# Kernel optimization log

Hardware: AMD Instinct MI355X
Metric: run time of the kernel (lower is better)

The kernel has to match this reference:

```python
import jax, jax.numpy as jnp
import numpy as np

N = 100_000      # nodes
E = 1_600_000    # edges (avg degree 16)
D_IN, D_H, D_OUT = 128, 128, 64


def setup_inputs() -> dict:
    key = jax.random.key(0)
    ks = jax.random.split(key, 6)
    x = jax.random.normal(ks[0], (N, D_IN), jnp.float32)
    edge_index = jax.random.randint(ks[1], (2, E), 0, N, dtype=jnp.int32)
    W1 = jax.random.normal(ks[2], (D_IN, D_H), jnp.float32) / np.sqrt(D_IN)
    b1 = jnp.zeros((D_H,), jnp.float32)
    W2 = jax.random.normal(ks[3], (D_H, D_OUT), jnp.float32) / np.sqrt(D_H)
    b2 = jnp.zeros((D_OUT,), jnp.float32)
    return {"x": x, "edge_index": edge_index, "W1": W1, "b1": b1, "W2": W2, "b2": b2}


def _gcn_layer(x, W, b, src, dst, n_nodes):
    # PyG GCNConv: h = x @ W; symmetric norm with self-loops; scatter-add; + bias
    h = x @ W                                        # [N, D_out]
    deg = jax.ops.segment_sum(jnp.ones_like(dst, jnp.float32), dst,
                              num_segments=n_nodes)  # self-loops => deg >= 1
    dinv = jax.lax.rsqrt(deg)                        # deg^{-1/2}
    norm = dinv[src] * dinv[dst]                     # [E+N]
    msg = h[src] * norm[:, None]                     # gather + scale
    out = jax.ops.segment_sum(msg, dst, num_segments=n_nodes)  # scatter-add
    return out + b


def reference(x, edge_index, W1, b1, W2, b2):
    n = x.shape[0]
    loop = jnp.arange(n, dtype=edge_index.dtype)
    src = jnp.concatenate([edge_index[0], loop])     # add self-loops
    dst = jnp.concatenate([edge_index[1], loop])
    h = _gcn_layer(x, W1, b1, src, dst, n)
    h = jax.nn.relu(h)
    # dropout(p=0.5) is identity in eval mode
    out = _gcn_layer(h, W2, b2, src, dst, n)
    return out
```

## Files before the change

kernel.cpp:

```cpp
#include <hip/hip_runtime.h>
#include <hip/hip_bf16.h>


#define NTHREADS 256
#define BSH 8
#define NBMAX 512
#define FC_CAP 8192

typedef unsigned int uint;
typedef unsigned short ushort;
typedef __attribute__((ext_vector_type(8))) short short8;
typedef __attribute__((ext_vector_type(4))) float floatx4;

__device__ __forceinline__ uint pack_bf16(float a, float b) {
    __hip_bfloat162 h = __float22bfloat162_rn(make_float2(a, b));
    return *reinterpret_cast<uint*>(&h);
}
__device__ __forceinline__ float bf16_lo(uint q) { return __uint_as_float(q << 16); }
__device__ __forceinline__ float bf16_hi(uint q) { return __uint_as_float(q & 0xffff0000u); }

__global__ __launch_bounds__(256) void bucket_hist_kernel(
    const int* __restrict__ dst, int* __restrict__ bcnt, int e, int nb) {
    __shared__ int hist[NBMAX];
    int t = threadIdx.x;
    for (int b = t; b < nb; b += 256) hist[b] = 0;
    __syncthreads();
    int e0 = blockIdx.x * 2048;
#pragma unroll
    for (int v = 0; v < 2; v++) {
        int gi = e0 + t * 8 + v * 4;
        if (gi + 3 < e) {
            int4 d4 = *(const int4*)&dst[gi];
            atomicAdd(&hist[d4.x >> BSH], 1);
            atomicAdd(&hist[d4.y >> BSH], 1);
            atomicAdd(&hist[d4.z >> BSH], 1);
            atomicAdd(&hist[d4.w >> BSH], 1);
        } else {
            for (int j = 0; j < 4; j++)
                if (gi + j < e) atomicAdd(&hist[dst[gi + j] >> BSH], 1);
        }
    }
    __syncthreads();
    for (int b = t; b < nb; b += 256) {
        int v = hist[b];
        if (v) atomicAdd(&bcnt[b], v);
    }
}

__global__ void bucket_scan(const int* __restrict__ bcnt, int* __restrict__ bstart,
                            int* __restrict__ bcursor, int nb) {
    __shared__ int buf[NBMAX];
    int t = threadIdx.x;
    int v = (t < nb) ? bcnt[t] : 0;
    buf[t] = v;
    __syncthreads();
    int x = v;
    for (int off = 1; off < NBMAX; off <<= 1) {
        int y = (t >= off) ? buf[t - off] : 0;
        __syncthreads();
        x += y;
        buf[t] = x;
        __syncthreads();
    }
    if (t < nb) {
        bstart[t] = x - v;
        bcursor[t] = x - v;
    }
}

__global__ __launch_bounds__(256) void partition_kernel(
    const int* __restrict__ src, const int* __restrict__ dst,
    int* __restrict__ bcursor, uint* __restrict__ staged, int e, int nb) {
    __shared__ uint eP[2048];
    __shared__ ushort eB[2048];
    __shared__ int hist[NBMAX];
    __shared__ int base[NBMAX];
    int t = threadIdx.x;
    int e0 = blockIdx.x * 2048;

    for (int b = t; b < nb; b += 256) hist[b] = 0;
    __syncthreads();
#pragma unroll
    for (int v = 0; v < 2; v++) {
        int li = t * 8 + v * 4;
        int gi = e0 + li;
        int4 s4, d4;
        if (gi + 3 < e) {
            s4 = *(const int4*)&src[gi];
            d4 = *(const int4*)&dst[gi];
        } else {
            const int* sp = &src[gi];
            const int* dp = &dst[gi];
            s4.x = (gi + 0 < e) ? sp[0] : 0;  d4.x = (gi + 0 < e) ? dp[0] : -1;
            s4.y = (gi + 1 < e) ? sp[1] : 0;  d4.y = (gi + 1 < e) ? dp[1] : -1;
            s4.z = (gi + 2 < e) ? sp[2] : 0;  d4.z = (gi + 2 < e) ? dp[2] : -1;
            s4.w = (gi + 3 < e) ? sp[3] : 0;  d4.w = (gi + 3 < e) ? dp[3] : -1;
        }
        uint4 p4;
        p4.x = ((uint)s4.x << 8) | ((uint)d4.x & 255u);
        p4.y = ((uint)s4.y << 8) | ((uint)d4.y & 255u);
        p4.z = ((uint)s4.z << 8) | ((uint)d4.z & 255u);
        p4.w = ((uint)s4.w << 8) | ((uint)d4.w & 255u);
        *(uint4*)&eP[li] = p4;
        eB[li + 0] = (d4.x >= 0) ? (ushort)(d4.x >> BSH) : (ushort)0xFFFF;
        eB[li + 1] = (d4.y >= 0) ? (ushort)(d4.y >> BSH) : (ushort)0xFFFF;
        eB[li + 2] = (d4.z >= 0) ? (ushort)(d4.z >> BSH) : (ushort)0xFFFF;
        eB[li + 3] = (d4.w >= 0) ? (ushort)(d4.w >> BSH) : (ushort)0xFFFF;
        if (d4.x >= 0) atomicAdd(&hist[d4.x >> BSH], 1);
        if (d4.y >= 0) atomicAdd(&hist[d4.y >> BSH], 1);
        if (d4.z >= 0) atomicAdd(&hist[d4.z >> BSH], 1);
        if (d4.w >= 0) atomicAdd(&hist[d4.w >> BSH], 1);
    }
    __syncthreads();
    for (int b = t; b < nb; b += 256) {
        int v = hist[b];
        base[b] = v ? atomicAdd(&bcursor[b], v) : 0;
        hist[b] = 0;
    }
    __syncthreads();
#pragma unroll
    for (int i = 0; i < 8; i++) {
        int li = t + i * 256;
        ushort bb = eB[li];
        if (bb != (ushort)0xFFFF) {
            int r = atomicAdd(&hist[bb], 1);
            staged[base[bb] + r] = eP[li];
        }
    }
}

__global__ __launch_bounds__(256) void fine_csr_kernel(
    const uint* __restrict__ staged, const int* __restrict__ bstart,
    const int* __restrict__ bcnt, int4* __restrict__ meta,
    float* __restrict__ dinv, int* __restrict__ rec, int n) {
    __shared__ uint eL[FC_CAP];
    __shared__ int lcnt[256];
    __shared__ int tsum[256];
    int b = blockIdx.x;
    int t = threadIdx.x;
    lcnt[t] = 0;
    __syncthreads();
    int s0 = bstart[b];
    int m = bcnt[b];
    for (int i = t; i < m; i += 256) {
        uint pk = staged[s0 + i];
        if (i < FC_CAP) eL[i] = pk;
        atomicAdd(&lcnt[pk & 255u], 1);
    }
    __syncthreads();
    int v = lcnt[t];
    tsum[t] = v;
    __syncthreads();
    int x = v;
    for (int off = 1; off < 256; off <<= 1) {
        int y = (t >= off) ? tsum[t - off] : 0;
        __syncthreads();
        x += y;
        tsum[t] = x;
        __syncthreads();
    }
    int excl = x - v;
    int node = (b << BSH) + t;
    if (node < n) {
        float di = rsqrtf((float)v + 1.0f);
        dinv[node] = di;
        meta[node] = make_int4(s0 + excl, v, __float_as_int(di), __float_as_int(di * di));
    }
    lcnt[t] = s0 + excl;
    __syncthreads();
    for (int i = t; i < m; i += 256) {
        uint pk = (i < FC_CAP) ? eL[i] : staged[s0 + i];
        int pos = atomicAdd(&lcnt[pk & 255u], 1);
        rec[pos] = (int)(pk >> 8);
    }
}

template <int COLS, bool XF32>
__global__ __launch_bounds__(256) void gemm_mfma(const void* __restrict__ Xv,
                                                 const float* __restrict__ W,
                                                 uint* __restrict__ Cq,
                                                 const float* __restrict__ dscale,
                                                 int n) {
    __shared__ ushort sX[64 * 128];
    __shared__ ushort sWT[COLS * 128];
    int t = threadIdx.x;
    int rbase = blockIdx.x * 64;

    if (XF32) {
        const float* X = (const float*)Xv;
#pragma unroll
        for (int i = 0; i < 8; i++) {
            int f = t + 256 * i;
            int r = f >> 5;
            int c4 = f & 31;
            float4 v = make_float4(0.f, 0.f, 0.f, 0.f);
            int gr = rbase + r;
            if (gr < n) v = *(const float4*)(X + (size_t)gr * 128 + c4 * 4);
            uint lo = pack_bf16(v.x, v.y);
            uint hi = pack_bf16(v.z, v.w);
            int chunk = c4 >> 1;
            int sub = (c4 & 1) * 4;
            int off = r * 128 + (((chunk ^ (r & 15)) << 3) + sub);
            *(uint2*)&sX[off] = make_uint2(lo, hi);
        }
    } else {
        const ushort* X = (const ushort*)Xv;
#pragma unroll
        for (int i = 0; i < 4; i++) {
            int f = t + 256 * i;
            int r = f >> 4;
            int chunk = f & 15;
            uint4 v = make_uint4(0, 0, 0, 0);
            int gr = rbase + r;
            if (gr < n) v = *(const uint4*)(X + (size_t)gr * 128 + chunk * 8);
            int off = r * 128 + ((chunk ^ (r & 15)) << 3);
            *(uint4*)&sX[off] = v;
        }
    }
    {
        constexpr int UNITS = 64 * (COLS / 4);
        constexpr int PER_T = UNITS / 256;
#pragma unroll
        for (int i = 0; i < PER_T; i++) {
            int u = t + 256 * i;
            int kp = u / (COLS / 4);
            int n4 = u % (COLS / 4);
            int k = kp * 2;
            float4 w0 = *(const float4*)(W + (size_t)k * COLS + n4 * 4);
            float4 w1 = *(const float4*)(W + (size_t)(k + 1) * COLS + n4 * 4);
            int chunk = k >> 3;
            int sub = k & 7;
            const float* a0 = (const float*)&w0;
            const float* a1 = (const float*)&w1;
#pragma unroll
            for (int j = 0; j < 4; j++) {
                int nn = n4 * 4 + j;
                uint pk = pack_bf16(a0[j], a1[j]);
                int off = nn * 128 + (((chunk ^ (nn & 15)) << 3) + sub);
                *(uint*)&sWT[off] = pk;
            }
        }
    }
    __syncthreads();

    int lane = t & 63;
    int wave = t >> 6;
    int m = lane & 15;
    int q = lane >> 4;
    int r0 = wave * 16;

    floatx4 acc[COLS / 16];
#pragma unroll
    for (int c = 0; c < COLS / 16; c++) acc[c] = (floatx4){0.f, 0.f, 0.f, 0.f};

#pragma unroll
    for (int ks = 0; ks < 4; ks++) {
        int rr = r0 + m;
        int ca = (ks * 4 + q) ^ (rr & 15);
        short8 afrag = *(const short8*)&sX[rr * 128 + (ca << 3)];
#pragma unroll
        for (int c = 0; c < COLS / 16; c++) {
            int nn = c * 16 + m;
            int cb = (ks * 4 + q) ^ (nn & 15);
            short8 bfrag = *(const short8*)&sWT[nn * 128 + (cb << 3)];
            acc[c] = __builtin_amdgcn_mfma_f32_16x16x32_bf16(bfrag, afrag, acc[c], 0, 0, 0);
        }
    }

    int gr = rbase + r0 + m;
    if (gr < n) {
        float sc = dscale[gr];
#pragma unroll
        for (int c = 0; c < COLS / 16; c++) {
            uint2 pk;
            pk.x = pack_bf16(acc[c][0] * sc, acc[c][1] * sc);
            pk.y = pack_bf16(acc[c][2] * sc, acc[c][3] * sc);
            *(uint2*)&Cq[(size_t)gr * (COLS / 2) + c * 8 + q * 2] = pk;
        }
    }
}

__global__ __launch_bounds__(512) void agg128_mm64(
    const uint* __restrict__ hq, const int* __restrict__ rec,
    const int4* __restrict__ meta, const float* __restrict__ dinv,
    const float* __restrict__ bias, const float* __restrict__ W2,
    uint* __restrict__ h2q, int n) {
    __shared__ ushort sWT[64 * 128];
    __shared__ ushort sg[32 * 128];
    int t = threadIdx.x;

#pragma unroll
    for (int i = 0; i < 2; i++) {
        int u = t + 512 * i;
        int kp = u >> 4;
        int n4 = u & 15;
        int k = kp * 2;
        float4 w0 = *(const float4*)(W2 + (size_t)k * 64 + n4 * 4);
        float4 w1 = *(const float4*)(W2 + (size_t)(k + 1) * 64 + n4 * 4);
        int chunk = k >> 3;
        int sub = k & 7;
        const float* a0f = (const float*)&w0;
        const float* a1f = (const float*)&w1;
#pragma unroll
        for (int j = 0; j < 4; j++) {
            int nn = n4 * 4 + j;
            uint pk = pack_bf16(a0f[j], a1f[j]);
            *(uint*)&sWT[nn * 128 + (((chunk ^ (nn & 15)) << 3) + sub)] = pk;
        }
    }

    int qw = t >> 4;
    int fl = t & 15;
    int nb0 = blockIdx.x * 32;
    int w = nb0 + qw;
    bool valid = w < n;
    int wsafe = valid ? w : 0;
    const uint4* h4 = (const uint4*)hq;

    int4 mt = meta[wsafe];
    int j0 = mt.x;
    int deg = valid ? mt.y : 0;
    float di = __int_as_float(mt.z);

    uint4 qs = h4[(size_t)wsafe * 16 + fl];
    float a0 = bf16_lo(qs.x), a1 = bf16_hi(qs.x);
    float a2 = bf16_lo(qs.y), a3 = bf16_hi(qs.y);
    float a4 = bf16_lo(qs.z), a5 = bf16_hi(qs.z);
    float a6 = bf16_lo(qs.w), a7 = bf16_hi(qs.w);
    if (!valid) { a0 = a1 = a2 = a3 = a4 = a5 = a6 = a7 = 0.f; }

    const int* rp = rec + j0;
    int tt = 0;
    for (; tt + 8 <= deg; tt += 8) {
        int s[8]; uint4 q[8];
#pragma unroll
        for (int u = 0; u < 8; u++) s[u] = rp[tt + u];
#pragma unroll
        for (int u = 0; u < 8; u++) q[u] = h4[(size_t)s[u] * 16 + fl];
#pragma unroll
        for (int u = 0; u < 8; u++) {
            a0 += bf16_lo(q[u].x); a1 += bf16_hi(q[u].x);
            a2 += bf16_lo(q[u].y); a3 += bf16_hi(q[u].y);
            a4 += bf16_lo(q[u].z); a5 += bf16_hi(q[u].z);
            a6 += bf16_lo(q[u].w); a7 += bf16_hi(q[u].w);
        }
    }
    for (; tt + 2 <= deg; tt += 2) {
        int s0i = rp[tt], s1i = rp[tt + 1];
        uint4 q0 = h4[(size_t)s0i * 16 + fl];
        uint4 q1 = h4[(size_t)s1i * 16 + fl];
        a0 += bf16_lo(q0.x) + bf16_lo(q1.x);
        a1 += bf16_hi(q0.x) + bf16_hi(q1.x);
        a2 += bf16_lo(q0.y) + bf16_lo(q1.y);
        a3 += bf16_hi(q0.y) + bf16_hi(q1.y);
        a4 += bf16_lo(q0.z) + bf16_lo(q1.z);
        a5 += bf16_hi(q0.z) + bf16_hi(q1.z);
        a6 += bf16_lo(q0.w) + bf16_lo(q1.w);
        a7 += bf16_hi(q0.w) + bf16_hi(q1.w);
    }
    if (tt < deg) {
        int s = rp[tt];
        uint4 q0 = h4[(size_t)s * 16 + fl];
        a0 += bf16_lo(q0.x); a1 += bf16_hi(q0.x);
        a2 += bf16_lo(q0.y); a3 += bf16_hi(q0.y);
        a4 += bf16_lo(q0.z); a5 += bf16_hi(q0.z);
        a6 += bf16_lo(q0.w); a7 += bf16_hi(q0.w);
    }

    float4 bb0 = *(const float4*)&bias[8 * fl];
    float4 bb1 = *(const float4*)&bias[8 * fl + 4];
    uint4 pkv;
    pkv.x = pack_bf16(fmaxf(di * a0 + bb0.x, 0.f), fmaxf(di * a1 + bb0.y, 0.f));
    pkv.y = pack_bf16(fmaxf(di * a2 + bb0.z, 0.f), fmaxf(di * a3 + bb0.w, 0.f));
    pkv.z = pack_bf16(fmaxf(di * a4 + bb1.x, 0.f), fmaxf(di * a5 + bb1.y, 0.f));
    pkv.w = pack_bf16(fmaxf(di * a6 + bb1.z, 0.f), fmaxf(di * a7 + bb1.w, 0.f));
    *(uint4*)&sg[qw * 128 + ((fl ^ (qw & 15)) << 3)] = pkv;
    __syncthreads();

    int wave = t >> 6;
    int lane = t & 63;
    int m = lane & 15;
    int qq = lane >> 4;
    int rt = wave >> 2;
    int ct = wave & 3;
    floatx4 acc = (floatx4){0.f, 0.f, 0.f, 0.f};
#pragma unroll
    for (int ks = 0; ks < 4; ks++) {
        int rr = rt * 16 + m;
        int ca = (ks * 4 + qq) ^ (rr & 15);
        short8 afrag = *(const short8*)&sg[rr * 128 + (ca << 3)];
        int nn = ct * 16 + m;
        int cb = (ks * 4 + qq) ^ (nn & 15);
        short8 bfrag = *(const short8*)&sWT[nn * 128 + (cb << 3)];
        acc = __builtin_amdgcn_mfma_f32_16x16x32_bf16(bfrag, afrag, acc, 0, 0, 0);
    }
    int gr = nb0 + rt * 16 + m;
    if (gr < n) {
        float sc = dinv[gr];
        uint2 pk;
        pk.x = pack_bf16(acc[0] * sc, acc[1] * sc);
        pk.y = pack_bf16(acc[2] * sc, acc[3] * sc);
        *(uint2*)&h2q[(size_t)gr * 32 + ct * 8 + qq * 2] = pk;
    }
}

__global__ __launch_bounds__(256) void aggregate64q(
    const uint* __restrict__ hq, const int* __restrict__ rec,
    const int4* __restrict__ meta, const float* __restrict__ bias,
    float* __restrict__ out, int n) {
    int gt = blockIdx.x * 256 + threadIdx.x;
    int w = gt >> 3;
    if (w >= n) return;
    int fl = gt & 7;

    int4 mt = meta[w];
    int j0 = mt.x;
    int deg = mt.y;
    float di = __int_as_float(mt.z);
    const uint4* h4 = (const uint4*)hq;

    uint4 qs = h4[(size_t)w * 8 + fl];
    float a0 = bf16_lo(qs.x), a1 = bf16_hi(qs.x);
    float a2 = bf16_lo(qs.y), a3 = bf16_hi(qs.y);
    float a4 = bf16_lo(qs.z), a5 = bf16_hi(qs.z);
    float a6 = bf16_lo(qs.w), a7 = bf16_hi(qs.w);

    const int* rp = rec + j0;
    int tt = 0;
    for (; tt + 8 <= deg; tt += 8) {
        int s[8]; uint4 q[8];
#pragma unroll
        for (int u = 0; u < 8; u++) s[u] = rp[tt + u];
#pragma unroll
        for (int u = 0; u < 8; u++) q[u] = h4[(size_t)s[u] * 8 + fl];
#pragma unroll
        for (int u = 0; u < 8; u++) {
            a0 += bf16_lo(q[u].x); a1 += bf16_hi(q[u].x);
            a2 += bf16_lo(q[u].y); a3 += bf16_hi(q[u].y);
            a4 += bf16_lo(q[u].z); a5 += bf16_hi(q[u].z);
            a6 += bf16_lo(q[u].w); a7 += bf16_hi(q[u].w);
        }
    }
    for (; tt + 2 <= deg; tt += 2) {
        int s0i = rp[tt], s1i = rp[tt + 1];
        uint4 q0 = h4[(size_t)s0i * 8 + fl];
        uint4 q1 = h4[(size_t)s1i * 8 + fl];
        a0 += bf16_lo(q0.x) + bf16_lo(q1.x);
        a1 += bf16_hi(q0.x) + bf16_hi(q1.x);
        a2 += bf16_lo(q0.y) + bf16_lo(q1.y);
        a3 += bf16_hi(q0.y) + bf16_hi(q1.y);
        a4 += bf16_lo(q0.z) + bf16_lo(q1.z);
        a5 += bf16_hi(q0.z) + bf16_hi(q1.z);
        a6 += bf16_lo(q0.w) + bf16_lo(q1.w);
        a7 += bf16_hi(q0.w) + bf16_hi(q1.w);
    }
    if (tt < deg) {
        int s = rp[tt];
        uint4 q0 = h4[(size_t)s * 8 + fl];
        a0 += bf16_lo(q0.x); a1 += bf16_hi(q0.x);
        a2 += bf16_lo(q0.y); a3 += bf16_hi(q0.y);
        a4 += bf16_lo(q0.z); a5 += bf16_hi(q0.z);
        a6 += bf16_lo(q0.w); a7 += bf16_hi(q0.w);
    }

    float4 bb0 = *(const float4*)&bias[8 * fl];
    float4 bb1 = *(const float4*)&bias[8 * fl + 4];
    float4 o0, o1;
    o0.x = di * a0 + bb0.x; o0.y = di * a1 + bb0.y;
    o0.z = di * a2 + bb0.z; o0.w = di * a3 + bb0.w;
    o1.x = di * a4 + bb1.x; o1.y = di * a5 + bb1.y;
    o1.z = di * a6 + bb1.z; o1.w = di * a7 + bb1.w;
    *(float4*)&out[(size_t)w * 64 + 8 * fl] = o0;
    *(float4*)&out[(size_t)w * 64 + 8 * fl + 4] = o1;
}

extern "C" void kernel_launch(void* const* d_in, const int* in_sizes, int n_in,
                              void* d_out, int out_size, void* d_ws, size_t ws_size,
                              hipStream_t stream) {
    const float* x = (const float*)d_in[0];
    const int* edge = (const int*)d_in[1];
    const float* W1 = (const float*)d_in[2];
    const float* b1 = (const float*)d_in[3];
    const float* W2 = (const float*)d_in[4];
    const float* b2 = (const float*)d_in[5];

    const int N = in_sizes[0] / 128;
    const int E = in_sizes[1] / 2;
    const int* src = edge;
    const int* dst = edge + E;
    const int NB = (N + (1 << BSH) - 1) >> BSH;

    char* p = (char*)d_ws;
    int* bcnt = (int*)p;      p += NBMAX * 4;
    int* bstart = (int*)p;    p += NBMAX * 4;
    int* bcursor = (int*)p;   p += NBMAX * 4;
    float* dinv = (float*)p;  p += (size_t)N * 4;
    int4* meta = (int4*)p;    p += (size_t)N * 16;
    int* rec = (int*)p;       p += (size_t)E * 4;
    uint* staged = (uint*)p;  p += (size_t)E * 4;
    uint* hq = (uint*)p;      p += (size_t)N * 64 * 4;
    uint* h2q = (uint*)p;     p += (size_t)N * 32 * 4;

    float* out = (float*)d_out;
    const int eblocks = (E + 2047) / 2048;

    (void)hipMemsetAsync(bcnt, 0, NBMAX * 4, stream);
    bucket_hist_kernel<<<eblocks, 256, 0, stream>>>(dst, bcnt, E, NB);
    bucket_scan<<<1, NBMAX, 0, stream>>>(bcnt, bstart, bcursor, NB);
    partition_kernel<<<eblocks, 256, 0, stream>>>(src, dst, bcursor, staged, E, NB);
    fine_csr_kernel<<<NB, 256, 0, stream>>>(staged, bstart, bcnt, meta, dinv, rec, N);

    const int gblocks = (N + 63) / 64;

    gemm_mfma<128, true><<<gblocks, 256, 0, stream>>>(x, W1, hq, dinv, N);
    agg128_mm64<<<(N + 31) / 32, 512, 0, stream>>>(hq, rec, meta, dinv, b1, W2, h2q, N);
    aggregate64q<<<(N * 8 + 255) / 256, 256, 0, stream>>>(h2q, rec, meta, b2, out, N);
}
```

Baseline: 294.3 us.

## Split aggregation feature halves across XCD groups with persistent work queues

```diff
diff --git a/kernel.cpp b/kernel.cpp
--- a/kernel.cpp
+++ b/kernel.cpp
@@ -18,6 +18,12 @@
 }
 __device__ __forceinline__ float bf16_lo(uint q) { return __uint_as_float(q << 16); }
 __device__ __forceinline__ float bf16_hi(uint q) { return __uint_as_float(q & 0xffff0000u); }
+
+__device__ __forceinline__ int xcd_id() {
+    uint x;
+    asm volatile("s_getreg_b32 %0, hwreg(HW_REG_XCC_ID)" : "=s"(x));
+    return (int)(x & 7u);
+}
 
 __global__ __launch_bounds__(256) void bucket_hist_kernel(
     const int* __restrict__ dst, int* __restrict__ bcnt, int e, int nb) {
@@ -280,198 +286,187 @@
     }
 }
 
-__global__ __launch_bounds__(512) void agg128_mm64(
-    const uint* __restrict__ hq, const int* __restrict__ rec,
-    const int4* __restrict__ meta, const float* __restrict__ dinv,
-    const float* __restrict__ bias, const float* __restrict__ W2,
-    uint* __restrict__ h2q, int n) {
-    __shared__ ushort sWT[64 * 128];
-    __shared__ ushort sg[32 * 128];
-    int t = threadIdx.x;
-
-#pragma unroll
-    for (int i = 0; i < 2; i++) {
-        int u = t + 512 * i;
-        int kp = u >> 4;
-        int n4 = u & 15;
-        int k = kp * 2;
-        float4 w0 = *(const float4*)(W2 + (size_t)k * 64 + n4 * 4);
-        float4 w1 = *(const float4*)(W2 + (size_t)(k + 1) * 64 + n4 * 4);
-        int chunk = k >> 3;
-        int sub = k & 7;
-        const float* a0f = (const float*)&w0;
-        const float* a1f = (const float*)&w1;
-#pragma unroll
-        for (int j = 0; j < 4; j++) {
-            int nn = n4 * 4 + j;
-            uint pk = pack_bf16(a0f[j], a1f[j]);
-            *(uint*)&sWT[nn * 128 + (((chunk ^ (nn & 15)) << 3) + sub)] = pk;
-        }
-    }
-
-    int qw = t >> 4;
-    int fl = t & 15;
-    int nb0 = blockIdx.x * 32;
-    int w = nb0 + qw;
-    bool valid = w < n;
-    int wsafe = valid ? w : 0;
-    const uint4* h4 = (const uint4*)hq;
-
-    int4 mt = meta[wsafe];
-    int j0 = mt.x;
-    int deg = valid ? mt.y : 0;
-    float di = __int_as_float(mt.z);
-
-    uint4 qs = h4[(size_t)wsafe * 16 + fl];
-    float a0 = bf16_lo(qs.x), a1 = bf16_hi(qs.x);
-    float a2 = bf16_lo(qs.y), a3 = bf16_hi(qs.y);
-    float a4 = bf16_lo(qs.z), a5 = bf16_hi(qs.z);
-    float a6 = bf16_lo(qs.w), a7 = bf16_hi(qs.w);
-    if (!valid) { a0 = a1 = a2 = a3 = a4 = a5 = a6 = a7 = 0.f; }
-
-    const int* rp = rec + j0;
-    int tt = 0;
-    for (; tt + 8 <= deg; tt += 8) {
-        int s[8]; uint4 q[8];
-#pragma unroll
-        for (int u = 0; u < 8; u++) s[u] = rp[tt + u];
-#pragma unroll
-        for (int u = 0; u < 8; u++) q[u] = h4[(size_t)s[u] * 16 + fl];
-#pragma unroll
-        for (int u = 0; u < 8; u++) {
-            a0 += bf16_lo(q[u].x); a1 += bf16_hi(q[u].x);
-            a2 += bf16_lo(q[u].y); a3 += bf16_hi(q[u].y);
-            a4 += bf16_lo(q[u].z); a5 += bf16_hi(q[u].z);
-            a6 += bf16_lo(q[u].w); a7 += bf16_hi(q[u].w);
-        }
-    }
-    for (; tt + 2 <= deg; tt += 2) {
-        int s0i = rp[tt], s1i = rp[tt + 1];
-        uint4 q0 = h4[(size_t)s0i * 16 + fl];
-        uint4 q1 = h4[(size_t)s1i * 16 + fl];
-        a0 += bf16_lo(q0.x) + bf16_lo(q1.x);
-        a1 += bf16_hi(q0.x) + bf16_hi(q1.x);
-        a2 += bf16_lo(q0.y) + bf16_lo(q1.y);
-        a3 += bf16_hi(q0.y) + bf16_hi(q1.y);
-        a4 += bf16_lo(q0.z) + bf16_lo(q1.z);
-        a5 += bf16_hi(q0.z) + bf16_hi(q1.z);
-        a6 += bf16_lo(q0.w) + bf16_lo(q1.w);
-        a7 += bf16_hi(q0.w) + bf16_hi(q1.w);
-    }
-    if (tt < deg) {
-        int s = rp[tt];
-        uint4 q0 = h4[(size_t)s * 16 + fl];
-        a0 += bf16_lo(q0.x); a1 += bf16_hi(q0.x);
-        a2 += bf16_lo(q0.y); a3 += bf16_hi(q0.y);
-        a4 += bf16_lo(q0.z); a5 += bf16_hi(q0.z);
-        a6 += bf16_lo(q0.w); a7 += bf16_hi(q0.w);
-    }
-
-    float4 bb0 = *(const float4*)&bias[8 * fl];
-    float4 bb1 = *(const float4*)&bias[8 * fl + 4];
-    uint4 pkv;
-    pkv.x = pack_bf16(fmaxf(di * a0 + bb0.x, 0.f), fmaxf(di * a1 + bb0.y, 0.f));
-    pkv.y = pack_bf16(fmaxf(di * a2 + bb0.z, 0.f), fmaxf(di * a3 + bb0.w, 0.f));
-    pkv.z = pack_bf16(fmaxf(di * a4 + bb1.x, 0.f), fmaxf(di * a5 + bb1.y, 0.f));
-    pkv.w = pack_bf16(fmaxf(di * a6 + bb1.z, 0.f), fmaxf(di * a7 + bb1.w, 0.f));
-    *(uint4*)&sg[qw * 128 + ((fl ^ (qw & 15)) << 3)] = pkv;
-    __syncthreads();
-
-    int wave = t >> 6;
-    int lane = t & 63;
-    int m = lane & 15;
-    int qq = lane >> 4;
-    int rt = wave >> 2;
-    int ct = wave & 3;
-    floatx4 acc = (floatx4){0.f, 0.f, 0.f, 0.f};
-#pragma unroll
-    for (int ks = 0; ks < 4; ks++) {
-        int rr = rt * 16 + m;
-        int ca = (ks * 4 + qq) ^ (rr & 15);
-        short8 afrag = *(const short8*)&sg[rr * 128 + (ca << 3)];
-        int nn = ct * 16 + m;
-        int cb = (ks * 4 + qq) ^ (nn & 15);
-        short8 bfrag = *(const short8*)&sWT[nn * 128 + (cb << 3)];
-        acc = __builtin_amdgcn_mfma_f32_16x16x32_bf16(bfrag, afrag, acc, 0, 0, 0);
-    }
-    int gr = nb0 + rt * 16 + m;
-    if (gr < n) {
-        float sc = dinv[gr];
-        uint2 pk;
-        pk.x = pack_bf16(acc[0] * sc, acc[1] * sc);
-        pk.y = pack_bf16(acc[2] * sc, acc[3] * sc);
-        *(uint2*)&h2q[(size_t)gr * 32 + ct * 8 + qq * 2] = pk;
-    }
-}
-
-__global__ __launch_bounds__(256) void aggregate64q(
+__global__ __launch_bounds__(512) void agg128h(
     const uint* __restrict__ hq, const int* __restrict__ rec,
     const int4* __restrict__ meta, const float* __restrict__ bias,
-    float* __restrict__ out, int n) {
-    int gt = blockIdx.x * 256 + threadIdx.x;
-    int w = gt >> 3;
-    if (w >= n) return;
-    int fl = gt & 7;
-
-    int4 mt = meta[w];
-    int j0 = mt.x;
-    int deg = mt.y;
-    float di = __int_as_float(mt.z);
+    int* __restrict__ wcur, uint* __restrict__ gq, int n) {
+    __shared__ int2 sWk;
+    int t = threadIdx.x;
+    const int NG = (n + 63) >> 6;
+    int myhf = (xcd_id() >> 2) & 1;
     const uint4* h4 = (const uint4*)hq;
 
-    uint4 qs = h4[(size_t)w * 8 + fl];
-    float a0 = bf16_lo(qs.x), a1 = bf16_hi(qs.x);
-    float a2 = bf16_lo(qs.y), a3 = bf16_hi(qs.y);
-    float a4 = bf16_lo(qs.z), a5 = bf16_hi(qs.z);
-    float a6 = bf16_lo(qs.w), a7 = bf16_hi(qs.w);
-
-    const int* rp = rec + j0;
-    int tt = 0;
-    for (; tt + 8 <= deg; tt += 8) {
-        int s[8]; uint4 q[8];
-#pragma unroll
-        for (int u = 0; u < 8; u++) s[u] = rp[tt + u];
-#pragma unroll
-        for (int u = 0; u < 8; u++) q[u] = h4[(size_t)s[u] * 8 + fl];
-#pragma unroll
-        for (int u = 0; u < 8; u++) {
-            a0 += bf16_lo(q[u].x); a1 += bf16_hi(q[u].x);
-            a2 += bf16_lo(q[u].y); a3 += bf16_hi(q[u].y);
-            a4 += bf16_lo(q[u].z); a5 += bf16_hi(q[u].z);
-            a6 += bf16_lo(q[u].w); a7 += bf16_hi(q[u].w);
-        }
-    }
-    for (; tt + 2 <= deg; tt += 2) {
-        int s0i = rp[tt], s1i = rp[tt + 1];
-        uint4 q0 = h4[(size_t)s0i * 8 + fl];
-        uint4 q1 = h4[(size_t)s1i * 8 + fl];
-        a0 += bf16_lo(q0.x) + bf16_lo(q1.x);
-        a1 += bf16_hi(q0.x) + bf16_hi(q1.x);
-        a2 += bf16_lo(q0.y) + bf16_lo(q1.y);
-        a3 += bf16_hi(q0.y) + bf16_hi(q1.y);
-        a4 += bf16_lo(q0.z) + bf16_lo(q1.z);
-        a5 += bf16_hi(q0.z) + bf16_hi(q1.z);
-        a6 += bf16_lo(q0.w) + bf16_lo(q1.w);
-        a7 += bf16_hi(q0.w) + bf16_hi(q1.w);
-    }
-    if (tt < deg) {
-        int s = rp[tt];
-        uint4 q0 = h4[(size_t)s * 8 + fl];
-        a0 += bf16_lo(q0.x); a1 += bf16_hi(q0.x);
-        a2 += bf16_lo(q0.y); a3 += bf16_hi(q0.y);
-        a4 += bf16_lo(q0.z); a5 += bf16_hi(q0.z);
-        a6 += bf16_lo(q0.w); a7 += bf16_hi(q0.w);
-    }
-
-    float4 bb0 = *(const float4*)&bias[8 * fl];
-    float4 bb1 = *(const float4*)&bias[8 * fl + 4];
-    float4 o0, o1;
-    o0.x = di * a0 + bb0.x; o0.y = di * a1 + bb0.y;
-    o0.z = di * a2 + bb0.z; o0.w = di * a3 + bb0.w;
-    o1.x = di * a4 + bb1.x; o1.y = di * a5 + bb1.y;
-    o1.z = di * a6 + bb1.z; o1.w = di * a7 + bb1.w;
-    *(float4*)&out[(size_t)w * 64 + 8 * fl] = o0;
-    *(float4*)&out[(size_t)w * 64 + 8 * fl + 4] = o1;
+    for (;;) {
+        if (t == 0) {
+            int h = myhf;
+            int g = atomicAdd(&wcur[h], 1);
+            if (g >= NG) { h ^= 1; g = atomicAdd(&wcur[h], 1); }
+            sWk = make_int2(h, g);
+        }
+        __syncthreads();
+        int hf = sWk.x;
+        int ng = sWk.y;
+        __syncthreads();
+        if (ng >= NG) break;
+
+        int w = (ng << 6) + (t >> 3);
+        int fl = t & 7;
+        bool valid = w < n;
+        int ws = valid ? w : 0;
+        int4 mt = meta[ws];
+        int j0 = mt.x;
+        int deg = valid ? mt.y : 0;
+        float di = __int_as_float(mt.z);
+        int off = hf * 8 + fl;
+
+        uint4 qs = h4[(size_t)ws * 16 + off];
+        float a0 = bf16_lo(qs.x), a1 = bf16_hi(qs.x);
+        float a2 = bf16_lo(qs.y), a3 = bf16_hi(qs.y);
+        float a4 = bf16_lo(qs.z), a5 = bf16_hi(qs.z);
+        float a6 = bf16_lo(qs.w), a7 = bf16_hi(qs.w);
+
+        const int* rp = rec + j0;
+        int tt = 0;
+        for (; tt + 8 <= deg; tt += 8) {
+            int s[8]; uint4 q[8];
+#pragma unroll
+            for (int u = 0; u < 8; u++) s[u] = rp[tt + u];
+#pragma unroll
+            for (int u = 0; u < 8; u++) q[u] = h4[(size_t)s[u] * 16 + off];
+#pragma unroll
+            for (int u = 0; u < 8; u++) {
+                a0 += bf16_lo(q[u].x); a1 += bf16_hi(q[u].x);
+                a2 += bf16_lo(q[u].y); a3 += bf16_hi(q[u].y);
+                a4 += bf16_lo(q[u].z); a5 += bf16_hi(q[u].z);
+                a6 += bf16_lo(q[u].w); a7 += bf16_hi(q[u].w);
+            }
+        }
+        for (; tt + 2 <= deg; tt += 2) {
+            int s0i = rp[tt], s1i = rp[tt + 1];
+            uint4 q0 = h4[(size_t)s0i * 16 + off];
+            uint4 q1 = h4[(size_t)s1i * 16 + off];
+            a0 += bf16_lo(q0.x) + bf16_lo(q1.x);
+            a1 += bf16_hi(q0.x) + bf16_hi(q1.x);
+            a2 += bf16_lo(q0.y) + bf16_lo(q1.y);
+            a3 += bf16_hi(q0.y) + bf16_hi(q1.y);
+            a4 += bf16_lo(q0.z) + bf16_lo(q1.z);
+            a5 += bf16_hi(q0.z) + bf16_hi(q1.z);
+            a6 += bf16_lo(q0.w) + bf16_lo(q1.w);
+            a7 += bf16_hi(q0.w) + bf16_hi(q1.w);
+        }
+        if (tt < deg) {
+            int s = rp[tt];
+            uint4 q0 = h4[(size_t)s * 16 + off];
+            a0 += bf16_lo(q0.x); a1 += bf16_hi(q0.x);
+            a2 += bf16_lo(q0.y); a3 += bf16_hi(q0.y);
+            a4 += bf16_lo(q0.z); a5 += bf16_hi(q0.z);
+            a6 += bf16_lo(q0.w); a7 += bf16_hi(q0.w);
+        }
+
+        if (valid) {
+            int fb = hf * 64 + 8 * fl;
+            float4 bb0 = *(const float4*)&bias[fb];
+            float4 bb1 = *(const float4*)&bias[fb + 4];
+            uint4 pkv;
+            pkv.x = pack_bf16(fmaxf(di * a0 + bb0.x, 0.f), fmaxf(di * a1 + bb0.y, 0.f));
+            pkv.y = pack_bf16(fmaxf(di * a2 + bb0.z, 0.f), fmaxf(di * a3 + bb0.w, 0.f));
+            pkv.z = pack_bf16(fmaxf(di * a4 + bb1.x, 0.f), fmaxf(di * a5 + bb1.y, 0.f));
+            pkv.w = pack_bf16(fmaxf(di * a6 + bb1.z, 0.f), fmaxf(di * a7 + bb1.w, 0.f));
+            ((uint4*)gq)[(size_t)w * 16 + off] = pkv;
+        }
+    }
+}
+
+__global__ __launch_bounds__(512) void agg64h(
+    const uint* __restrict__ h2q, const int* __restrict__ rec,
+    const int4* __restrict__ meta, const float* __restrict__ bias,
+    int* __restrict__ wcur, float* __restrict__ out, int n) {
+    __shared__ int2 sWk;
+    int t = threadIdx.x;
+    const int NG = (n + 127) >> 7;
+    int myhf = (xcd_id() >> 2) & 1;
+    const uint4* h4 = (const uint4*)h2q;
+
+    for (;;) {
+        if (t == 0) {
+            int h = myhf;
+            int g = atomicAdd(&wcur[h], 1);
+            if (g >= NG) { h ^= 1; g = atomicAdd(&wcur[h], 1); }
+            sWk = make_int2(h, g);
+        }
+        __syncthreads();
+        int hf = sWk.x;
+        int ng = sWk.y;
+        __syncthreads();
+        if (ng >= NG) break;
+
+        int w = (ng << 7) + (t >> 2);
+        int fl = t & 3;
+        bool valid = w < n;
+        int ws = valid ? w : 0;
+        int4 mt = meta[ws];
+        int j0 = mt.x;
+        int deg = valid ? mt.y : 0;
+        float di = __int_as_float(mt.z);
+        int off = hf * 4 + fl;
+
+        uint4 qs = h4[(size_t)ws * 8 + off];
+        float a0 = bf16_lo(qs.x), a1 = bf16_hi(qs.x);
+        float a2 = bf16_lo(qs.y), a3 = bf16_hi(qs.y);
+        float a4 = bf16_lo(qs.z), a5 = bf16_hi(qs.z);
+        float a6 = bf16_lo(qs.w), a7 = bf16_hi(qs.w);
+
+        const int* rp = rec + j0;
+        int tt = 0;
+        for (; tt + 8 <= deg; tt += 8) {
+            int s[8]; uint4 q[8];
+#pragma unroll
+            for (int u = 0; u < 8; u++) s[u] = rp[tt + u];
+#pragma unroll
+            for (int u = 0; u < 8; u++) q[u] = h4[(size_t)s[u] * 8 + off];
+#pragma unroll
+            for (int u = 0; u < 8; u++) {
+                a0 += bf16_lo(q[u].x); a1 += bf16_hi(q[u].x);
+                a2 += bf16_lo(q[u].y); a3 += bf16_hi(q[u].y);
+                a4 += bf16_lo(q[u].z); a5 += bf16_hi(q[u].z);
+                a6 += bf16_lo(q[u].w); a7 += bf16_hi(q[u].w);
+            }
+        }
+        for (; tt + 2 <= deg; tt += 2) {
+            int s0i = rp[tt], s1i = rp[tt + 1];
+            uint4 q0 = h4[(size_t)s0i * 8 + off];
+            uint4 q1 = h4[(size_t)s1i * 8 + off];
+            a0 += bf16_lo(q0.x) + bf16_lo(q1.x);
+            a1 += bf16_hi(q0.x) + bf16_hi(q1.x);
+            a2 += bf16_lo(q0.y) + bf16_lo(q1.y);
+            a3 += bf16_hi(q0.y) + bf16_hi(q1.y);
+            a4 += bf16_lo(q0.z) + bf16_lo(q1.z);
+            a5 += bf16_hi(q0.z) + bf16_hi(q1.z);
+            a6 += bf16_lo(q0.w) + bf16_lo(q1.w);
+            a7 += bf16_hi(q0.w) + bf16_hi(q1.w);
+        }
+        if (tt < deg) {
+            int s = rp[tt];
+            uint4 q0 = h4[(size_t)s * 8 + off];
+            a0 += bf16_lo(q0.x); a1 += bf16_hi(q0.x);
+            a2 += bf16_lo(q0.y); a3 += bf16_hi(q0.y);
+            a4 += bf16_lo(q0.z); a5 += bf16_hi(q0.z);
+            a6 += bf16_lo(q0.w); a7 += bf16_hi(q0.w);
+        }
+
+        if (valid) {
+            int fb = hf * 32 + 8 * fl;
+            float4 bb0 = *(const float4*)&bias[fb];
+            float4 bb1 = *(const float4*)&bias[fb + 4];
+            float4 o0, o1;
+            o0.x = di * a0 + bb0.x; o0.y = di * a1 + bb0.y;
+            o0.z = di * a2 + bb0.z; o0.w = di * a3 + bb0.w;
+            o1.x = di * a4 + bb1.x; o1.y = di * a5 + bb1.y;
+            o1.z = di * a6 + bb1.z; o1.w = di * a7 + bb1.w;
+            *(float4*)&out[(size_t)w * 64 + fb] = o0;
+            *(float4*)&out[(size_t)w * 64 + fb + 4] = o1;
+        }
+    }
 }
 
 extern "C" void kernel_launch(void* const* d_in, const int* in_sizes, int n_in,
@@ -494,17 +489,20 @@
     int* bcnt = (int*)p;      p += NBMAX * 4;
     int* bstart = (int*)p;    p += NBMAX * 4;
     int* bcursor = (int*)p;   p += NBMAX * 4;
+    int* wcur = (int*)p;      p += 16;
     float* dinv = (float*)p;  p += (size_t)N * 4;
     int4* meta = (int4*)p;    p += (size_t)N * 16;
     int* rec = (int*)p;       p += (size_t)E * 4;
     uint* staged = (uint*)p;  p += (size_t)E * 4;
     uint* hq = (uint*)p;      p += (size_t)N * 64 * 4;
+    uint* gq = (uint*)p;      p += (size_t)N * 64 * 4;
     uint* h2q = (uint*)p;     p += (size_t)N * 32 * 4;
 
     float* out = (float*)d_out;
     const int eblocks = (E + 2047) / 2048;
 
     (void)hipMemsetAsync(bcnt, 0, NBMAX * 4, stream);
+    (void)hipMemsetAsync(wcur, 0, 16, stream);
     bucket_hist_kernel<<<eblocks, 256, 0, stream>>>(dst, bcnt, E, NB);
     bucket_scan<<<1, NBMAX, 0, stream>>>(bcnt, bstart, bcursor, NB);
     partition_kernel<<<eblocks, 256, 0, stream>>>(src, dst, bcursor, staged, E, NB);
@@ -513,6 +511,7 @@
     const int gblocks = (N + 63) / 64;
 
     gemm_mfma<128, true><<<gblocks, 256, 0, stream>>>(x, W1, hq, dinv, N);
-    agg128_mm64<<<(N + 31) / 32, 512, 0, stream>>>(hq, rec, meta, dinv, b1, W2, h2q, N);
-    aggregate64q<<<(N * 8 + 255) / 256, 256, 0, stream>>>(h2q, rec, meta, b2, out, N);
-}
+    agg128h<<<1024, 512, 0, stream>>>(hq, rec, meta, b1, wcur, gq, N);
+    gemm_mfma<64, false><<<gblocks, 256, 0, stream>>>(gq, W2, h2q, dinv, N);
+    agg64h<<<1024, 512, 0, stream>>>(h2q, rec, meta, b2, wcur + 2, out, N);
+}
```

New measurement: 433.8 us. 47.4% more time.

## Replace bucket histogram and scan with fixed-capacity bucket staging

Applied to the files above, without the earlier changes.

```diff
diff --git a/kernel.cpp b/kernel.cpp
--- a/kernel.cpp
+++ b/kernel.cpp
@@ -5,6 +5,7 @@
 #define NTHREADS 256
 #define BSH 8
 #define NBMAX 512
+#define BCAP 5632
 #define FC_CAP 8192
 
 typedef unsigned int uint;
@@ -19,58 +20,9 @@
 __device__ __forceinline__ float bf16_lo(uint q) { return __uint_as_float(q << 16); }
 __device__ __forceinline__ float bf16_hi(uint q) { return __uint_as_float(q & 0xffff0000u); }
 
-__global__ __launch_bounds__(256) void bucket_hist_kernel(
-    const int* __restrict__ dst, int* __restrict__ bcnt, int e, int nb) {
-    __shared__ int hist[NBMAX];
-    int t = threadIdx.x;
-    for (int b = t; b < nb; b += 256) hist[b] = 0;
-    __syncthreads();
-    int e0 = blockIdx.x * 2048;
-#pragma unroll
-    for (int v = 0; v < 2; v++) {
-        int gi = e0 + t * 8 + v * 4;
-        if (gi + 3 < e) {
-            int4 d4 = *(const int4*)&dst[gi];
-            atomicAdd(&hist[d4.x >> BSH], 1);
-            atomicAdd(&hist[d4.y >> BSH], 1);
-            atomicAdd(&hist[d4.z >> BSH], 1);
-            atomicAdd(&hist[d4.w >> BSH], 1);
-        } else {
-            for (int j = 0; j < 4; j++)
-                if (gi + j < e) atomicAdd(&hist[dst[gi + j] >> BSH], 1);
-        }
-    }
-    __syncthreads();
-    for (int b = t; b < nb; b += 256) {
-        int v = hist[b];
-        if (v) atomicAdd(&bcnt[b], v);
-    }
-}
-
-__global__ void bucket_scan(const int* __restrict__ bcnt, int* __restrict__ bstart,
-                            int* __restrict__ bcursor, int nb) {
-    __shared__ int buf[NBMAX];
-    int t = threadIdx.x;
-    int v = (t < nb) ? bcnt[t] : 0;
-    buf[t] = v;
-    __syncthreads();
-    int x = v;
-    for (int off = 1; off < NBMAX; off <<= 1) {
-        int y = (t >= off) ? buf[t - off] : 0;
-        __syncthreads();
-        x += y;
-        buf[t] = x;
-        __syncthreads();
-    }
-    if (t < nb) {
-        bstart[t] = x - v;
-        bcursor[t] = x - v;
-    }
-}
-
 __global__ __launch_bounds__(256) void partition_kernel(
     const int* __restrict__ src, const int* __restrict__ dst,
-    int* __restrict__ bcursor, uint* __restrict__ staged, int e, int nb) {
+    int* __restrict__ bfill, uint* __restrict__ staged, int e, int nb) {
     __shared__ uint eP[2048];
     __shared__ ushort eB[2048];
     __shared__ int hist[NBMAX];
@@ -114,7 +66,7 @@
     __syncthreads();
     for (int b = t; b < nb; b += 256) {
         int v = hist[b];
-        base[b] = v ? atomicAdd(&bcursor[b], v) : 0;
+        base[b] = v ? (b * BCAP + atomicAdd(&bfill[b], v)) : 0;
         hist[b] = 0;
     }
     __syncthreads();
@@ -130,21 +82,32 @@
 }
 
 __global__ __launch_bounds__(256) void fine_csr_kernel(
-    const uint* __restrict__ staged, const int* __restrict__ bstart,
-    const int* __restrict__ bcnt, int4* __restrict__ meta,
-    float* __restrict__ dinv, int* __restrict__ rec, int n) {
+    const uint* __restrict__ staged, const int* __restrict__ bfill,
+    int4* __restrict__ meta, float* __restrict__ dinv,
+    int* __restrict__ rec, int n) {
     __shared__ uint eL[FC_CAP];
     __shared__ int lcnt[256];
     __shared__ int tsum[256];
+    __shared__ int red[256];
     int b = blockIdx.x;
     int t = threadIdx.x;
+
+    int part = 0;
+    for (int j = t; j < b; j += 256) part += bfill[j];
+    red[t] = part;
     lcnt[t] = 0;
     __syncthreads();
-    int s0 = bstart[b];
-    int m = bcnt[b];
+    for (int off = 128; off > 0; off >>= 1) {
+        if (t < off) red[t] += red[t + off];
+        __syncthreads();
+    }
+    int s0 = red[0];
+    int m = bfill[b];
+
+    int sb = b * BCAP;
     for (int i = t; i < m; i += 256) {
-        uint pk = staged[s0 + i];
-        if (i < FC_CAP) eL[i] = pk;
+        uint pk = staged[sb + i];
+        eL[i] = pk;
         atomicAdd(&lcnt[pk & 255u], 1);
     }
     __syncthreads();
@@ -169,7 +132,7 @@
     lcnt[t] = s0 + excl;
     __syncthreads();
     for (int i = t; i < m; i += 256) {
-        uint pk = (i < FC_CAP) ? eL[i] : staged[s0 + i];
+        uint pk = eL[i];
         int pos = atomicAdd(&lcnt[pk & 255u], 1);
         rec[pos] = (int)(pk >> 8);
     }
@@ -491,24 +454,20 @@
     const int NB = (N + (1 << BSH) - 1) >> BSH;
 
     char* p = (char*)d_ws;
-    int* bcnt = (int*)p;      p += NBMAX * 4;
-    int* bstart = (int*)p;    p += NBMAX * 4;
-    int* bcursor = (int*)p;   p += NBMAX * 4;
+    int* bfill = (int*)p;     p += NBMAX * 4;
     float* dinv = (float*)p;  p += (size_t)N * 4;
     int4* meta = (int4*)p;    p += (size_t)N * 16;
     int* rec = (int*)p;       p += (size_t)E * 4;
-    uint* staged = (uint*)p;  p += (size_t)E * 4;
+    uint* staged = (uint*)p;  p += (size_t)NBMAX * BCAP * 4;
     uint* hq = (uint*)p;      p += (size_t)N * 64 * 4;
     uint* h2q = (uint*)p;     p += (size_t)N * 32 * 4;
 
     float* out = (float*)d_out;
     const int eblocks = (E + 2047) / 2048;
 
-    (void)hipMemsetAsync(bcnt, 0, NBMAX * 4, stream);
-    bucket_hist_kernel<<<eblocks, 256, 0, stream>>>(dst, bcnt, E, NB);
-    bucket_scan<<<1, NBMAX, 0, stream>>>(bcnt, bstart, bcursor, NB);
-    partition_kernel<<<eblocks, 256, 0, stream>>>(src, dst, bcursor, staged, E, NB);
-    fine_csr_kernel<<<NB, 256, 0, stream>>>(staged, bstart, bcnt, meta, dinv, rec, N);
+    (void)hipMemsetAsync(bfill, 0, NBMAX * 4, stream);
+    partition_kernel<<<eblocks, 256, 0, stream>>>(src, dst, bfill, staged, E, NB);
+    fine_csr_kernel<<<NB, 256, 0, stream>>>(staged, bfill, meta, dinv, rec, N);
 
     const int gblocks = (N + 63) / 64;
 
```

Result: faster. 274.9 us (-6.6%).
